# Kernel optimization log

Hardware: AMD Instinct MI355X
Metric: run time of the kernel (lower is better)

The kernel has to match this reference:

```python
import jax, jax.numpy as jnp
import numpy as np

N_NODES = 40000
EMB = 256
NHEADS = 2
HEAD = EMB // NHEADS
NLAYERS = 4
NGNN = 2
LN_EPS = 1e-5
LEAKY = 0.01


def setup_inputs() -> dict:
    key = jax.random.key(0)
    ks = iter(jax.random.split(key, 40))
    nrm = lambda shape, s=0.05: jax.random.normal(next(ks), shape, dtype=jnp.float32) * s
    inp = {
        'feat0': nrm((20000, 512), 1.0),
        'feat1': nrm((20000, 512), 1.0),
        'fc_w0': nrm((256, 512)), 'fc_b0': jnp.zeros((256,), jnp.float32),
        'fc_w1': nrm((256, 512)), 'fc_b1': jnp.zeros((256,), jnp.float32),
        'gcn_w': nrm((NGNN, 256, 256)),
        'edge_src': jax.random.randint(next(ks), (640000,), 0, N_NODES),
        'edge_dst': jax.random.randint(next(ks), (640000,), 0, N_NODES),
        'dg_seqs': jax.random.randint(next(ks), (1024, 64), 0, N_NODES),
        'pt_seqs': jax.random.randint(next(ks), (1024, 64), 0, N_NODES),
        'type_emb': nrm((4, 4), 1.0),
        'node_type': jax.random.randint(next(ks), (N_NODES,), 0, 4),
        'gt_wl': nrm((8, 256, 256)), 'gt_wr': nrm((8, 256, 256)),
        'gt_al': nrm((8, 1, HEAD)), 'gt_ar': nrm((8, 1, HEAD)),
        'gt_wf': nrm((8, 256, 256)),
        'ln_g': jnp.ones((8, 256), jnp.float32), 'ln_b': jnp.zeros((8, 256), jnp.float32),
        'proj_d_w': nrm((2, 256, 256)), 'proj_d_b': jnp.zeros((2, 256), jnp.float32),
        'proj_p_w': nrm((2, 256, 256)), 'proj_p_b': jnp.zeros((2, 256), jnp.float32),
        'ml_w1': nrm((256, 512)), 'ml_b1': jnp.zeros((256,), jnp.float32),
        'ml_w2': nrm((128, 256)), 'ml_b2': jnp.zeros((128,), jnp.float32),
        'ml_w3': nrm((1, 128)), 'ml_b3': jnp.zeros((1,), jnp.float32),
    }
    return inp


def _layernorm(x, g, b):
    m = x.mean(-1, keepdims=True)
    v = ((x - m) ** 2).mean(-1, keepdims=True)
    return (x - m) * jax.lax.rsqrt(v + LN_EPS) * g + b


def _leaky(x):
    return jnp.where(x >= 0, x, LEAKY * x)


def _agt_layer(h, wl, wr, al, ar, wf, g, b):
    # h: [B, L, EMB]; additive (GAT-style) attention, temper = 1.0
    B, L, _ = h.shape
    fl = (h @ wl.T).reshape(B, L, NHEADS, HEAD).transpose(0, 2, 1, 3)  # [B,H,L,hd]
    fr = (h @ wr.T).reshape(B, L, NHEADS, HEAD).transpose(0, 2, 1, 3)
    sl = _leaky(fl) @ al.T                     # [B,H,L,1]
    sr = _leaky(fr) @ ar.T                     # [B,H,L,1]
    score = jax.nn.softmax(sl + sr.transpose(0, 1, 3, 2), axis=-1)  # [B,H,L,L]
    ctx = score @ fr                           # [B,H,L,hd]
    h_sa = ctx.transpose(0, 2, 1, 3).reshape(B, L, EMB)
    return _layernorm(h + h_sa @ wf.T, g, b)


def _gcn(gh, W, src, dst):
    # DGL GraphConv norm='both', allow_zero_in_degree, activation=relu
    ones = jnp.ones(src.shape[0], gh.dtype)
    deg_out = jnp.clip(jax.ops.segment_sum(ones, src, num_segments=N_NODES), 1.0)
    deg_in = jnp.clip(jax.ops.segment_sum(ones, dst, num_segments=N_NODES), 1.0)
    x = gh * (deg_out ** -0.5)[:, None]
    x = x @ W
    agg = jax.ops.segment_sum(x[src], dst, num_segments=N_NODES)
    return jax.nn.relu(agg * (deg_in ** -0.5)[:, None])


def reference(feat0, feat1, fc_w0, fc_b0, fc_w1, fc_b1, gcn_w, edge_src, edge_dst,
              dg_seqs, pt_seqs, type_emb, node_type, gt_wl, gt_wr, gt_al, gt_ar,
              gt_wf, ln_g, ln_b, proj_d_w, proj_d_b, proj_p_w, proj_p_b,
              ml_w1, ml_b1, ml_w2, ml_b2, ml_w3, ml_b3):
    # per-type input projections, concatenated along node dim
    h0 = feat0 @ fc_w0.T + fc_b0
    h1 = feat1 @ fc_w1.T + fc_b1
    gh = jnp.concatenate([h0, h1], axis=0)  # [N, EMB]
    r = type_emb[node_type]                 # computed but unused downstream (faithful)
    for layer in range(NGNN):
        gh = _gcn(gh, gcn_w[layer], edge_src, edge_dst)
    # graph transformer per node type (dropout = identity in eval)
    embs = []
    for t, seqs in ((0, dg_seqs), (1, pt_seqs)):
        h = gh[seqs]                        # [B, L, EMB]
        _ = r[seqs]
        for l in range(NLAYERS):
            i = t * NLAYERS + l
            h = _agt_layer(h, gt_wl[i], gt_wr[i], gt_al[i], gt_ar[i], gt_wf[i], ln_g[i], ln_b[i])
        embs.append(h[:, 0, :])
    dg_emb, pt_emb = embs
    # Proj heads: linear -> elu -> linear
    dg_emb = jax.nn.elu(dg_emb @ proj_d_w[0].T + proj_d_b[0]) @ proj_d_w[1].T + proj_d_b[1]
    pt_emb = jax.nn.elu(pt_emb @ proj_p_w[0].T + proj_p_b[0]) @ proj_p_w[1].T + proj_p_b[1]
    # Predict MLP on concat
    x = jnp.concatenate([dg_emb, pt_emb], axis=1)  # [B, 512]
    x = jax.nn.relu(x @ ml_w1.T + ml_b1)
    x = jax.nn.relu(x @ ml_w2.T + ml_b2)
    out = jax.nn.sigmoid(x @ ml_w3.T + ml_b3)
    return out.reshape(x.shape[0])
```

## Files before the change

### kernel.cpp

```cpp
#include <hip/hip_runtime.h>
#include <hip/hip_bf16.h>
#include <math.h>

typedef unsigned int u32;
typedef unsigned short u16;
typedef __attribute__((ext_vector_type(8))) short bf16x8;
typedef __attribute__((ext_vector_type(4))) float f32x4;

__device__ __forceinline__ float b2f(u16 u) { union { u32 i; float f; } c; c.i = ((u32)u) << 16; return c.f; }
__device__ __forceinline__ u16 f2b(float f) { __hip_bfloat16 h = __float2bfloat16(f); u16 r; __builtin_memcpy(&r, &h, 2); return r; }
__device__ __forceinline__ float b2f_lo(u32 w) { union { u32 i; float f; } c; c.i = w << 16; return c.f; }
__device__ __forceinline__ float b2f_hi(u32 w) { union { u32 i; float f; } c; c.i = w & 0xffff0000u; return c.f; }
__device__ __forceinline__ u32 pk2(float a, float b) { return (u32)f2b(a) | ((u32)f2b(b) << 16); }

__device__ __forceinline__ float wave_sum(float v) {
    #pragma unroll
    for (int off = 32; off > 0; off >>= 1) v += __shfl_xor(v, off, 64);
    return v;
}

template<int CTRL>
__device__ __forceinline__ float dpp_addf(float v) {
    int y = __builtin_amdgcn_update_dpp(0, __builtin_bit_cast(int, v), CTRL, 0xF, 0xF, true);
    return v + __builtin_bit_cast(float, y);
}
__device__ __forceinline__ float sum16_dpp(float v) {
    v = dpp_addf<0xB1>(v);
    v = dpp_addf<0x4E>(v);
    v = dpp_addf<0x141>(v);
    v = dpp_addf<0x140>(v);
    return v;
}
__device__ __forceinline__ float sum8_dpp(float v) {
    v = dpp_addf<0xB1>(v);
    v = dpp_addf<0x4E>(v);
    v = dpp_addf<0x141>(v);
    return v;
}

template<bool AF32>
__global__ __launch_bounds__(256) void mfma_gemm_kernel(
    const void* __restrict__ Av, const u16* __restrict__ B,
    const float* __restrict__ bias, const float* __restrict__ rowscale,
    u16* __restrict__ Cb, int M, int N, int K,
    const void* __restrict__ Av1, const u16* __restrict__ B1,
    const float* __restrict__ bias1, u16* __restrict__ Cb1)
{
    if (blockIdx.z) { Av = Av1; B = B1; bias = bias1; Cb = Cb1; }
    __shared__ u16 lds[(64 + 128) * 64];
    const int tid = threadIdx.x;
    const int wid = tid >> 6, lane = tid & 63;
    const int wr = wid >> 1, wc = wid & 1;
    const int m0 = blockIdx.y * 64, n0 = blockIdx.x * 128;

    f32x4 acc[2][4] = {};

    for (int k0 = 0; k0 < K; k0 += 64) {
        #pragma unroll
        for (int s = 0; s < 2; ++s) {
            int idx = tid + s * 256;
            int row = idx >> 3, g = idx & 7;
            int row_g = m0 + row; if (row_g >= M) row_g = M - 1;
            int swz = ((g << 4) ^ ((row & 7) << 4));
            if (AF32) {
                const float* src = (const float*)Av + (size_t)row_g * K + k0 + g * 8;
                float4 v0 = *(const float4*)src;
                float4 v1 = *(const float4*)(src + 4);
                uint4 pk;
                pk.x = pk2(v0.x, v0.y); pk.y = pk2(v0.z, v0.w);
                pk.z = pk2(v1.x, v1.y); pk.w = pk2(v1.z, v1.w);
                *(uint4*)((char*)lds + row * 128 + swz) = pk;
            } else {
                f32x4 v = *(const f32x4*)((const u16*)Av + (size_t)row_g * K + k0 + g * 8);
                *(f32x4*)((char*)lds + row * 128 + swz) = v;
            }
        }
        #pragma unroll
        for (int s = 0; s < 4; ++s) {
            int idx = tid + s * 256;
            int row = idx >> 3, g = idx & 7;
            int row_g = n0 + row; if (row_g >= N) row_g = N - 1;
            f32x4 v = *(const f32x4*)(B + (size_t)row_g * K + k0 + g * 8);
            *(f32x4*)((char*)lds + 8192 + row * 128 + ((g << 4) ^ ((row & 7) << 4))) = v;
        }
        __syncthreads();
        #pragma unroll
        for (int ks = 0; ks < 2; ++ks) {
            const int off = (ks * 64 + ((lane >> 4) << 4)) ^ ((lane & 7) << 4);
            const int ra = lane & 15;
            bf16x8 af[2], bfr[4];
            #pragma unroll
            for (int i = 0; i < 2; ++i)
                af[i] = *(bf16x8*)((char*)lds + (wr * 32 + i * 16 + ra) * 128 + off);
            #pragma unroll
            for (int j = 0; j < 4; ++j)
                bfr[j] = *(bf16x8*)((char*)lds + 8192 + (wc * 64 + j * 16 + ra) * 128 + off);
            #pragma unroll
            for (int i = 0; i < 2; ++i)
                #pragma unroll
                for (int j = 0; j < 4; ++j)
                    acc[i][j] = __builtin_amdgcn_mfma_f32_16x16x32_bf16(af[i], bfr[j], acc[i][j], 0, 0, 0);
        }
        __syncthreads();
    }

    const int cr = lane >> 4, ccol = lane & 15;
    #pragma unroll
    for (int i = 0; i < 2; ++i) {
        #pragma unroll
        for (int j = 0; j < 4; ++j) {
            int colg = n0 + wc * 64 + j * 16 + ccol;
            if (colg >= N) continue;
            float badd = bias ? bias[colg] : 0.f;
            #pragma unroll
            for (int reg = 0; reg < 4; ++reg) {
                int rowg = m0 + wr * 32 + i * 16 + cr * 4 + reg;
                if (rowg >= M) continue;
                float v = acc[i][j][reg] + badd;
                if (rowscale) v *= rowscale[rowg];
                Cb[(size_t)rowg * N + colg] = f2b(v);
            }
        }
    }
}

__global__ __launch_bounds__(512, 4) void fused_transformer_kernel(
    const float* __restrict__ gh, const int* __restrict__ dg_seqs,
    const int* __restrict__ pt_seqs,
    const u16* __restrict__ wrN,
    const u32* __restrict__ wfT2,
    const float* __restrict__ ar,
    const float* __restrict__ lng, const float* __restrict__ lnb,
    float* __restrict__ embT)
{
    __shared__ u16 ldsA[64 * 256];
    __shared__ float scoreH[2][64];
    __shared__ float ctxS[256];
    __shared__ float uS[2][256];

    const int tid = threadIdx.x;
    const int bx = blockIdx.x;
    const int t = bx >> 10, s = bx & 1023;
    const int r = tid >> 3, o8 = tid & 7;
    const int wid = tid >> 6, lane = tid & 63;
    const int hd = wid >> 2;
    const int g4 = lane >> 4, cl = lane & 15;

    const int* seqs = t ? pt_seqs : dg_seqs;

    float4 y[8];
    {
        int node = seqs[s * 64 + r];
        const float* src = gh + (size_t)node * 256 + o8 * 32;
        #pragma unroll
        for (int v = 0; v < 8; ++v) y[v] = *(const float4*)(src + v * 4);
    }

    for (int l = 0; l < 4; ++l) {
        const int li = t * 4 + l;
        {
            const int c = o8 >> 1, gb = (o8 & 1) * 4;
            #pragma unroll
            for (int gg = 0; gg < 4; ++gg) {
                float4 a = y[2 * gg], b = y[2 * gg + 1];
                uint4 pk;
                pk.x = pk2(a.x, a.y); pk.y = pk2(a.z, a.w);
                pk.z = pk2(b.x, b.y); pk.w = pk2(b.z, b.w);
                int g = gb + gg;
                *(uint4*)((char*)ldsA + c * 8192 + r * 128 + ((g << 4) ^ ((r & 7) << 4))) = pk;
            }
            if (tid < 128) ((float*)scoreH)[tid] = 0.f;
        }
        __syncthreads();

        f32x4 acc[4][2] = {};
        {
            const u16* wrl = wrN + (size_t)li * 65536;
            const int ra = lane & 15;
            #pragma unroll
            for (int kc = 0; kc < 8; ++kc) {
                const int c = kc >> 1, ks = kc & 1;
                const int off = (ks * 64 + ((lane >> 4) << 4)) ^ ((lane & 7) << 4);
                bf16x8 af[4], bfr[2];
                #pragma unroll
                for (int i = 0; i < 4; ++i)
                    af[i] = *(bf16x8*)((char*)ldsA + c * 8192 + (i * 16 + ra) * 128 + off);
                #pragma unroll
                for (int j = 0; j < 2; ++j)
                    bfr[j] = *(const bf16x8*)(wrl + ((size_t)((wid * 2 + j) * 8 + kc) << 9) + lane * 8);
                #pragma unroll
                for (int i = 0; i < 4; ++i)
                    #pragma unroll
                    for (int j = 0; j < 2; ++j)
                        acc[i][j] = __builtin_amdgcn_mfma_f32_16x16x32_bf16(af[i], bfr[j], acc[i][j], 0, 0, 0);
            }
        }

        {
            const float* arl = ar + li * 128;
            float arj[2];
            #pragma unroll
            for (int j = 0; j < 2; ++j) arj[j] = arl[(wid & 3) * 32 + j * 16 + cl];
            #pragma unroll
            for (int i = 0; i < 4; ++i)
                #pragma unroll
                for (int reg = 0; reg < 4; ++reg) {
                    float sc;
                    {
                        float x0 = acc[i][0][reg], x1 = acc[i][1][reg];
                        sc = (x0 >= 0.f ? x0 : 0.01f * x0) * arj[0]
                           + (x1 >= 0.f ? x1 : 0.01f * x1) * arj[1];
                    }
                    sc = sum16_dpp(sc);
                    if (cl == 0) atomicAdd(&scoreH[hd][i * 16 + g4 * 4 + reg], sc);
                }
        }
        __syncthreads();

        float p[4][4];
        {
            const float* sc = scoreH[hd];
            #pragma unroll
            for (int i = 0; i < 4; ++i)
                *(float4*)p[i] = *(const float4*)(sc + i * 16 + g4 * 4);
            float mx = -1e30f;
            #pragma unroll
            for (int i = 0; i < 4; ++i)
                #pragma unroll
                for (int reg = 0; reg < 4; ++reg) mx = fmaxf(mx, p[i][reg]);
            mx = fmaxf(mx, __shfl_xor(mx, 16, 64));
            mx = fmaxf(mx, __shfl_xor(mx, 32, 64));
            float sme = 0.f;
            #pragma unroll
            for (int i = 0; i < 4; ++i)
                #pragma unroll
                for (int reg = 0; reg < 4; ++reg) {
                    p[i][reg] = __expf(p[i][reg] - mx);
                    sme += p[i][reg];
                }
            sme += __shfl_xor(sme, 16, 64);
            sme += __shfl_xor(sme, 32, 64);
            float inv = 1.f / sme;
            #pragma unroll
            for (int i = 0; i < 4; ++i)
                #pragma unroll
                for (int reg = 0; reg < 4; ++reg) p[i][reg] *= inv;
        }

        {
            #pragma unroll
            for (int j = 0; j < 2; ++j) {
                float c = 0.f;
                #pragma unroll
                for (int i = 0; i < 4; ++i)
                    #pragma unroll
                    for (int reg = 0; reg < 4; ++reg)
                        c = fmaf(p[i][reg], acc[i][j][reg], c);
                c += __shfl_xor(c, 16, 64);
                c += __shfl_xor(c, 32, 64);
                if (g4 == 0) ctxS[wid * 32 + j * 16 + cl] = c;
            }
        }
        __syncthreads();

        {
            const int n = tid & 255, half = tid >> 8;
            const u32* wp = wfT2 + (size_t)li * 32768 + (size_t)half * 16384 + n;
            const float* cx = ctxS + half * 128;
            float ua0 = 0.f, ua1 = 0.f, ua2 = 0.f, ua3 = 0.f;
            #pragma unroll 4
            for (int d2 = 0; d2 < 64; d2 += 4) {
                u32 w0 = wp[(size_t)(d2 + 0) * 256];
                u32 w1 = wp[(size_t)(d2 + 1) * 256];
                u32 w2 = wp[(size_t)(d2 + 2) * 256];
                u32 w3 = wp[(size_t)(d2 + 3) * 256];
                ua0 = fmaf(cx[2 * d2 + 0], b2f_lo(w0), ua0);
                ua0 = fmaf(cx[2 * d2 + 1], b2f_hi(w0), ua0);
                ua1 = fmaf(cx[2 * d2 + 2], b2f_lo(w1), ua1);
                ua1 = fmaf(cx[2 * d2 + 3], b2f_hi(w1), ua1);
                ua2 = fmaf(cx[2 * d2 + 4], b2f_lo(w2), ua2);
                ua2 = fmaf(cx[2 * d2 + 5], b2f_hi(w2), ua2);
                ua3 = fmaf(cx[2 * d2 + 6], b2f_lo(w3), ua3);
                ua3 = fmaf(cx[2 * d2 + 7], b2f_hi(w3), ua3);
            }
            uS[half][n] = (ua0 + ua1) + (ua2 + ua3);
        }
        __syncthreads();

        {
            #pragma unroll
            for (int v = 0; v < 8; ++v) {
                int c0 = o8 * 32 + v * 4;
                float4 u0 = *(const float4*)&uS[0][c0];
                float4 u1 = *(const float4*)&uS[1][c0];
                y[v].x += u0.x + u1.x; y[v].y += u0.y + u1.y;
                y[v].z += u0.z + u1.z; y[v].w += u0.w + u1.w;
            }
            float sm = 0.f, qq = 0.f;
            #pragma unroll
            for (int v = 0; v < 8; ++v) {
                sm += y[v].x + y[v].y + y[v].z + y[v].w;
                qq += y[v].x * y[v].x + y[v].y * y[v].y + y[v].z * y[v].z + y[v].w * y[v].w;
            }
            sm = sum8_dpp(sm);
            qq = sum8_dpp(qq);
            float mean = sm * (1.f / 256.f);
            float var = qq * (1.f / 256.f) - mean * mean;
            float inv = rsqrtf(var + 1e-5f);
            const float* gl = lng + li * 256 + o8 * 32;
            const float* bl = lnb + li * 256 + o8 * 32;
            if (l < 3) {
                #pragma unroll
                for (int v = 0; v < 8; ++v) {
                    float4 gv = *(const float4*)(gl + v * 4);
                    float4 bv = *(const float4*)(bl + v * 4);
                    y[v].x = (y[v].x - mean) * inv * gv.x + bv.x;
                    y[v].y = (y[v].y - mean) * inv * gv.y + bv.y;
                    y[v].z = (y[v].z - mean) * inv * gv.z + bv.z;
                    y[v].w = (y[v].w - mean) * inv * gv.w + bv.w;
                }
            } else if (r == 0) {
                float* dst = embT + (size_t)(t * 1024 + s) * 256 + o8 * 32;
                #pragma unroll
                for (int v = 0; v < 8; ++v) {
                    float4 gv = *(const float4*)(gl + v * 4);
                    float4 bv = *(const float4*)(bl + v * 4);
                    float4 o;
                    o.x = (y[v].x - mean) * inv * gv.x + bv.x;
                    o.y = (y[v].y - mean) * inv * gv.y + bv.y;
                    o.z = (y[v].z - mean) * inv * gv.z + bv.z;
                    o.w = (y[v].w - mean) * inv * gv.w + bv.w;
                    *(float4*)(dst + v * 4) = o;
                }
            }
        }
    }
}

template<bool BT>
__global__ __launch_bounds__(256) void gemm_kernel(
    const float* __restrict__ A, const float* __restrict__ B,
    const float* __restrict__ bias, const float* __restrict__ rowscale,
    float* __restrict__ C,
    int M, int N, int K, int lda, int ldb, int ldc, int coff, int act,
    const float* __restrict__ A1, const float* __restrict__ B1,
    const float* __restrict__ bias1, float* __restrict__ C1, int coff1)
{
    if (blockIdx.z) { A = A1; B = B1; bias = bias1; C = C1; coff = coff1; }
    __shared__ float As[32][64 + 4];
    __shared__ float Bs[32][64 + 4];
    const int tid = threadIdx.x;
    const int m0 = blockIdx.y * 64;
    const int n0 = blockIdx.x * 64;
    const int ty = tid >> 4, tx = tid & 15;
    float acc[4][4] = {};
    for (int k0 = 0; k0 < K; k0 += 32) {
        #pragma unroll
        for (int r = 0; r < 2; ++r) {
            int f4 = tid + r * 256;
            int arw = f4 >> 3, af = (f4 & 7) << 2;
            float4 v = make_float4(0.f, 0.f, 0.f, 0.f);
            int grow = m0 + arw;
            if (grow < M) {
                v = *(const float4*)(A + (size_t)grow * lda + k0 + af);
                if (rowscale) { float s = rowscale[grow]; v.x *= s; v.y *= s; v.z *= s; v.w *= s; }
            }
            As[af + 0][arw] = v.x; As[af + 1][arw] = v.y; As[af + 2][arw] = v.z; As[af + 3][arw] = v.w;
        }
        #pragma unroll
        for (int r = 0; r < 2; ++r) {
            int f4 = tid + r * 256;
            int col = f4 >> 3, kf = (f4 & 7) << 2;
            float4 v = make_float4(0.f, 0.f, 0.f, 0.f);
            if (n0 + col < N) v = *(const float4*)(B + (size_t)(n0 + col) * ldb + k0 + kf);
            Bs[kf + 0][col] = v.x; Bs[kf + 1][col] = v.y; Bs[kf + 2][col] = v.z; Bs[kf + 3][col] = v.w;
        }
        __syncthreads();
        #pragma unroll
        for (int kk = 0; kk < 32; ++kk) {
            float4 a4 = *(const float4*)&As[kk][ty << 2];
            float4 b4 = *(const float4*)&Bs[kk][tx << 2];
            float a[4] = {a4.x, a4.y, a4.z, a4.w};
            float b[4] = {b4.x, b4.y, b4.z, b4.w};
            #pragma unroll
            for (int i = 0; i < 4; ++i)
                #pragma unroll
                for (int j = 0; j < 4; ++j)
                    acc[i][j] = fmaf(a[i], b[j], acc[i][j]);
        }
        __syncthreads();
    }
    #pragma unroll
    for (int i = 0; i < 4; ++i) {
        int row = m0 + (ty << 2) + i;
        if (row >= M) continue;
        #pragma unroll
        for (int j = 0; j < 4; ++j) {
            int col = n0 + (tx << 2) + j;
            if (col >= N) continue;
            float v = acc[i][j];
            if (bias) v += bias[col];
            if (act == 1) v = fmaxf(v, 0.f);
            else if (act == 2) v = (v > 0.f) ? v : expm1f(v);
            C[(size_t)row * ldc + coff + col] = v;
        }
    }
}

__global__ __launch_bounds__(256) void conv_flat_kernel(const float* __restrict__ in, u16* __restrict__ out, int n) {
    int i = (blockIdx.x * 256 + threadIdx.x) * 4;
    if (i >= n) return;
    float4 v = *(const float4*)(in + i);
    *(uint2*)(out + i) = make_uint2(pk2(v.x, v.y), pk2(v.z, v.w));
}
__global__ __launch_bounds__(256) void conv_gcnw_kernel(const float* __restrict__ w, u16* __restrict__ out) {
    int idx = blockIdx.x * 256 + threadIdx.x;
    int l = blockIdx.y;
    int k = idx >> 8, n = idx & 255;
    out[(size_t)l * 65536 + n * 256 + k] = f2b(w[(size_t)l * 65536 + k * 256 + n]);
}
__global__ __launch_bounds__(256) void conv_wrN_kernel(const float* __restrict__ w, u16* __restrict__ out) {
    int idx = blockIdx.x * 256 + threadIdx.x;
    int lane = idx & 63;
    int kc = (idx >> 6) & 7;
    int gn = (idx >> 9) & 15;
    int l = idx >> 13;
    int row = gn * 16 + (lane & 15);
    int k0 = kc * 32 + (lane >> 4) * 8;
    const float* src = w + ((size_t)l * 256 + row) * 256 + k0;
    float4 v0 = *(const float4*)src;
    float4 v1 = *(const float4*)(src + 4);
    uint4 pk;
    pk.x = pk2(v0.x, v0.y); pk.y = pk2(v0.z, v0.w);
    pk.z = pk2(v1.x, v1.y); pk.w = pk2(v1.z, v1.w);
    *(uint4*)(out + (size_t)idx * 8) = pk;
}
__global__ __launch_bounds__(256) void conv_wfT2_kernel(const float* __restrict__ w, u32* __restrict__ out) {
    int idx = blockIdx.x * 256 + threadIdx.x;
    int n = idx & 255;
    int d2 = (idx >> 8) & 127;
    int l = idx >> 15;
    const float* src = w + ((size_t)l * 256 + n) * 256 + 2 * d2;
    out[idx] = pk2(src[0], src[1]);
}

#define EDGE_CAP 128
__global__ __launch_bounds__(256) void bucket_fill_kernel(
    const int* __restrict__ src, const int* __restrict__ dst,
    int* __restrict__ ebuf, int* __restrict__ cursor, int* __restrict__ cnt_out, int ne)
{
    int e0 = (blockIdx.x * 256 + threadIdx.x) * 4;
    if (e0 >= ne) return;
    int4 s4 = *(const int4*)(src + e0);
    int4 d4 = *(const int4*)(dst + e0);
    atomicAdd(&cnt_out[s4.x], 1);
    atomicAdd(&cnt_out[s4.y], 1);
    atomicAdd(&cnt_out[s4.z], 1);
    atomicAdd(&cnt_out[s4.w], 1);
    int p0 = atomicAdd(&cursor[d4.x], 1);
    int p1 = atomicAdd(&cursor[d4.y], 1);
    int p2 = atomicAdd(&cursor[d4.z], 1);
    int p3 = atomicAdd(&cursor[d4.w], 1);
    if (p0 < EDGE_CAP) ebuf[(size_t)d4.x * EDGE_CAP + p0] = s4.x;
    if (p1 < EDGE_CAP) ebuf[(size_t)d4.y * EDGE_CAP + p1] = s4.y;
    if (p2 < EDGE_CAP) ebuf[(size_t)d4.z * EDGE_CAP + p2] = s4.z;
    if (p3 < EDGE_CAP) ebuf[(size_t)d4.w * EDGE_CAP + p3] = s4.w;
}
__global__ __launch_bounds__(256) void deg_fin_kernel(const int* __restrict__ cnt, float* __restrict__ dinv, int n) {
    int i = blockIdx.x * 256 + threadIdx.x;
    if (i < n) dinv[i] = rsqrtf(fmaxf((float)cnt[i], 1.0f));
}

template<bool WF, bool WB>
__global__ __launch_bounds__(256) void csr_agg_kernel(
    const u16* __restrict__ x, const int* __restrict__ ebuf,
    const int* __restrict__ deg, float* __restrict__ outf, u16* __restrict__ outb, int nnodes)
{
    int n = blockIdx.x * 4 + (threadIdx.x >> 6);
    if (n >= nnodes) return;
    int lane = threadIdx.x & 63;
    int d = deg[n];
    float dinv = rsqrtf(fmaxf((float)d, 1.0f));
    if (d > EDGE_CAP) d = EDGE_CAP;
    const int* eb = ebuf + (size_t)n * EDGE_CAP;
    const int co = lane << 2;
    float a0 = 0.f, a1 = 0.f, a2 = 0.f, a3 = 0.f;
    int k = 0;
    for (; k + 4 <= d; k += 4) {
        int4 s4 = *(const int4*)(eb + k);
        uint2 va = *(const uint2*)(x + (size_t)s4.x * 256 + co);
        uint2 vb = *(const uint2*)(x + (size_t)s4.y * 256 + co);
        uint2 vc = *(const uint2*)(x + (size_t)s4.z * 256 + co);
        uint2 vd = *(const uint2*)(x + (size_t)s4.w * 256 + co);
        a0 += b2f_lo(va.x) + b2f_lo(vb.x) + b2f_lo(vc.x) + b2f_lo(vd.x);
        a1 += b2f_hi(va.x) + b2f_hi(vb.x) + b2f_hi(vc.x) + b2f_hi(vd.x);
        a2 += b2f_lo(va.y) + b2f_lo(vb.y) + b2f_lo(vc.y) + b2f_lo(vd.y);
        a3 += b2f_hi(va.y) + b2f_hi(vb.y) + b2f_hi(vc.y) + b2f_hi(vd.y);
    }
    for (; k < d; ++k) {
        int s = eb[k];
        uint2 v = *(const uint2*)(x + (size_t)s * 256 + co);
        a0 += b2f_lo(v.x); a1 += b2f_hi(v.x);
        a2 += b2f_lo(v.y); a3 += b2f_hi(v.y);
    }
    a0 = fmaxf(a0 * dinv, 0.f); a1 = fmaxf(a1 * dinv, 0.f);
    a2 = fmaxf(a2 * dinv, 0.f); a3 = fmaxf(a3 * dinv, 0.f);
    if (WF) *(float4*)(outf + (size_t)n * 256 + co) = make_float4(a0, a1, a2, a3);
    if (WB) *(uint2*)(outb + (size_t)n * 256 + co) = make_uint2(pk2(a0, a1), pk2(a2, a3));
}

__global__ __launch_bounds__(256) void final_kernel(
    const float* __restrict__ m2, const float* __restrict__ w3,
    const float* __restrict__ b3, float* __restrict__ out, int nrows)
{
    int row = blockIdx.x * 4 + (threadIdx.x >> 6);
    int lane = threadIdx.x & 63;
    if (row >= nrows) return;
    float s = m2[(size_t)row * 128 + lane] * w3[lane]
            + m2[(size_t)row * 128 + 64 + lane] * w3[64 + lane];
    s = wave_sum(s);
    if (lane == 0) out[row] = 1.f / (1.f + expf(-(s + b3[0])));
}

static inline int cdiv(int a, int b) { return (a + b - 1) / b; }

extern "C" void kernel_launch(void* const* d_in, const int* in_sizes, int n_in,
                              void* d_out, int out_size, void* d_ws, size_t ws_size,
                              hipStream_t stream)
{
    const float* feat0   = (const float*)d_in[0];
    const float* feat1   = (const float*)d_in[1];
    const float* fc_w0   = (const float*)d_in[2];
    const float* fc_b0   = (const float*)d_in[3];
    const float* fc_w1   = (const float*)d_in[4];
    const float* fc_b1   = (const float*)d_in[5];
    const float* gcn_w   = (const float*)d_in[6];
    const int*   edge_src= (const int*)d_in[7];
    const int*   edge_dst= (const int*)d_in[8];
    const int*   dg_seqs = (const int*)d_in[9];
    const int*   pt_seqs = (const int*)d_in[10];
    const float* gt_wr   = (const float*)d_in[14];
    const float* gt_ar   = (const float*)d_in[16];
    const float* gt_wf   = (const float*)d_in[17];
    const float* ln_g    = (const float*)d_in[18];
    const float* ln_b    = (const float*)d_in[19];
    const float* proj_d_w= (const float*)d_in[20];
    const float* proj_d_b= (const float*)d_in[21];
    const float* proj_p_w= (const float*)d_in[22];
    const float* proj_p_b= (const float*)d_in[23];
    const float* ml_w1   = (const float*)d_in[24];
    const float* ml_b1   = (const float*)d_in[25];
    const float* ml_w2   = (const float*)d_in[26];
    const float* ml_b2   = (const float*)d_in[27];
    const float* ml_w3   = (const float*)d_in[28];
    const float* ml_b3   = (const float*)d_in[29];
    float* out = (float*)d_out;

    float* base  = (float*)d_ws;
    float* gh    = base;
    float* gcnR  = gh + 10240000;
    float* dego  = gcnR + 15440000;
    float* embT  = dego + 40000;
    float* t1    = embT + 524288;
    float* mx    = t1 + 524288;
    float* m1    = mx + 524288;
    float* m2    = m1 + 262144;
    float* wreg  = m2 + 131072;

    u16* tmp_b   = (u16*)gcnR;
    int* ebuf    = (int*)(gcnR + 5120000);
    int* cursor  = ebuf + (size_t)40000 * EDGE_CAP;
    int* cnt_out = cursor + 40000;
    u16* gh_b    = (u16*)(gcnR + 10320000);

    u16* fcw_b   = (u16*)wreg;
    u16* gcnw_b  = fcw_b + 262144;
    u16* wrN     = gcnw_b + 131072;
    u32* wfT2    = (u32*)(wrN + 524288);

    conv_flat_kernel<<<cdiv(131072 / 4, 256), 256, 0, stream>>>(fc_w0, fcw_b, 131072);
    conv_flat_kernel<<<cdiv(131072 / 4, 256), 256, 0, stream>>>(fc_w1, fcw_b + 131072, 131072);
    conv_gcnw_kernel<<<dim3(256, 2), 256, 0, stream>>>(gcn_w, gcnw_b);
    conv_wrN_kernel<<<256, 256, 0, stream>>>(gt_wr, wrN);
    conv_wfT2_kernel<<<1024, 256, 0, stream>>>(gt_wf, wfT2);

    mfma_gemm_kernel<true><<<dim3(2, cdiv(20000, 64), 2), 256, 0, stream>>>(
        feat0, fcw_b, fc_b0, nullptr, gh_b, 20000, 256, 512,
        feat1, fcw_b + 131072, fc_b1, gh_b + (size_t)20000 * 256);

    hipMemsetAsync(cursor, 0, 80000 * sizeof(int), stream);
    bucket_fill_kernel<<<625, 256, 0, stream>>>(edge_src, edge_dst, ebuf, cursor, cnt_out, 640000);
    deg_fin_kernel<<<cdiv(40000, 256), 256, 0, stream>>>(cnt_out, dego, 40000);

    mfma_gemm_kernel<false><<<dim3(2, cdiv(40000, 64), 1), 256, 0, stream>>>(
        gh_b, gcnw_b, nullptr, dego, tmp_b, 40000, 256, 256,
        gh_b, gcnw_b, nullptr, tmp_b);
    csr_agg_kernel<false, true><<<10000, 256, 0, stream>>>(tmp_b, ebuf, cursor, gh, gh_b, 40000);
    mfma_gemm_kernel<false><<<dim3(2, cdiv(40000, 64), 1), 256, 0, stream>>>(
        gh_b, gcnw_b + 65536, nullptr, dego, tmp_b, 40000, 256, 256,
        gh_b, gcnw_b, nullptr, tmp_b);
    csr_agg_kernel<true, false><<<10000, 256, 0, stream>>>(tmp_b, ebuf, cursor, gh, gh_b, 40000);

    fused_transformer_kernel<<<2048, 512, 0, stream>>>(
        gh, dg_seqs, pt_seqs, wrN, wfT2, gt_ar, ln_g, ln_b, embT);

    gemm_kernel<true><<<dim3(4, 16, 2), 256, 0, stream>>>(
        embT, proj_d_w, proj_d_b, nullptr, t1, 1024, 256, 256, 256, 256, 256, 0, 2,
        embT + 262144, proj_p_w, proj_p_b, t1 + 262144, 0);
    gemm_kernel<true><<<dim3(4, 16, 2), 256, 0, stream>>>(
        t1, proj_d_w + 65536, proj_d_b + 256, nullptr, mx, 1024, 256, 256, 256, 256, 512, 0, 0,
        t1 + 262144, proj_p_w + 65536, proj_p_b + 256, mx, 256);

    gemm_kernel<true><<<dim3(4, 16, 1), 256, 0, stream>>>(
        mx, ml_w1, ml_b1, nullptr, m1, 1024, 256, 512, 512, 512, 256, 0, 1,
        mx, ml_w1, ml_b1, m1, 0);
    gemm_kernel<true><<<dim3(2, 16, 1), 256, 0, stream>>>(
        m1, ml_w2, ml_b2, nullptr, m2, 1024, 128, 256, 256, 256, 128, 0, 1,
        m1, ml_w2, ml_b2, m2, 0);
    final_kernel<<<256, 256, 0, stream>>>(m2, ml_w3, ml_b3, out, 1024);
}
```

Measured before the change: 651.1 us.

## Prefetch Wf weights, reswizzle LDS, merge conversion kernels, fuse MLP tail

The transformer kernel now prefetches the first 16 Wf weight words into registers at the start of each layer, so the loads overlap the QK/MFMA phase. It also adds a chunk-dependent XOR to the LDS swizzle and reads the context vector with float4 loads. Separately, five weight-conversion launches are merged into one kernel, and the last MLP GEMM and the sigmoid kernel are fused into a single tail kernel. These changes cut launch overhead and load latency at the cost of more register pressure in the main kernel.

```diff
diff --git a/kernel.cpp b/kernel.cpp
--- a/kernel.cpp
+++ b/kernel.cpp
@@ -147,6 +147,7 @@
     const int g4 = lane >> 4, cl = lane & 15;
 
     const int* seqs = t ? pt_seqs : dg_seqs;
+    const int un = tid & 255, uhalf = tid >> 8;
 
     float4 y[8];
     {
@@ -158,6 +159,12 @@
 
     for (int l = 0; l < 4; ++l) {
         const int li = t * 4 + l;
+        const u32* wp = wfT2 + (size_t)li * 32768 + (size_t)uhalf * 16384 + un;
+
+        u32 wpre[16];
+        #pragma unroll
+        for (int i = 0; i < 16; ++i) wpre[i] = wp[(size_t)i * 256];
+
         {
             const int c = o8 >> 1, gb = (o8 & 1) * 4;
             #pragma unroll
@@ -167,7 +174,8 @@
                 pk.x = pk2(a.x, a.y); pk.y = pk2(a.z, a.w);
                 pk.z = pk2(b.x, b.y); pk.w = pk2(b.z, b.w);
                 int g = gb + gg;
-                *(uint4*)((char*)ldsA + c * 8192 + r * 128 + ((g << 4) ^ ((r & 7) << 4))) = pk;
+                int off = ((g << 4) ^ ((r & 7) << 4)) ^ (c << 4);
+                *(uint4*)((char*)ldsA + c * 8192 + r * 128 + off) = pk;
             }
             if (tid < 128) ((float*)scoreH)[tid] = 0.f;
         }
@@ -180,7 +188,7 @@
             #pragma unroll
             for (int kc = 0; kc < 8; ++kc) {
                 const int c = kc >> 1, ks = kc & 1;
-                const int off = (ks * 64 + ((lane >> 4) << 4)) ^ ((lane & 7) << 4);
+                const int off = ((ks * 64 + ((lane >> 4) << 4)) ^ ((lane & 7) << 4)) ^ (c << 4);
                 bf16x8 af[4], bfr[2];
                 #pragma unroll
                 for (int i = 0; i < 4; ++i)
@@ -264,26 +272,31 @@
         __syncthreads();
 
         {
-            const int n = tid & 255, half = tid >> 8;
-            const u32* wp = wfT2 + (size_t)li * 32768 + (size_t)half * 16384 + n;
-            const float* cx = ctxS + half * 128;
+            const float* cx = ctxS + uhalf * 128;
             float ua0 = 0.f, ua1 = 0.f, ua2 = 0.f, ua3 = 0.f;
-            #pragma unroll 4
+            #pragma unroll
             for (int d2 = 0; d2 < 64; d2 += 4) {
-                u32 w0 = wp[(size_t)(d2 + 0) * 256];
-                u32 w1 = wp[(size_t)(d2 + 1) * 256];
-                u32 w2 = wp[(size_t)(d2 + 2) * 256];
-                u32 w3 = wp[(size_t)(d2 + 3) * 256];
-                ua0 = fmaf(cx[2 * d2 + 0], b2f_lo(w0), ua0);
-                ua0 = fmaf(cx[2 * d2 + 1], b2f_hi(w0), ua0);
-                ua1 = fmaf(cx[2 * d2 + 2], b2f_lo(w1), ua1);
-                ua1 = fmaf(cx[2 * d2 + 3], b2f_hi(w1), ua1);
-                ua2 = fmaf(cx[2 * d2 + 4], b2f_lo(w2), ua2);
-                ua2 = fmaf(cx[2 * d2 + 5], b2f_hi(w2), ua2);
-                ua3 = fmaf(cx[2 * d2 + 6], b2f_lo(w3), ua3);
-                ua3 = fmaf(cx[2 * d2 + 7], b2f_hi(w3), ua3);
-            }
-            uS[half][n] = (ua0 + ua1) + (ua2 + ua3);
+                u32 w0, w1, w2, w3;
+                if (d2 < 16) {
+                    w0 = wpre[d2]; w1 = wpre[d2 + 1]; w2 = wpre[d2 + 2]; w3 = wpre[d2 + 3];
+                } else {
+                    w0 = wp[(size_t)(d2 + 0) * 256];
+                    w1 = wp[(size_t)(d2 + 1) * 256];
+                    w2 = wp[(size_t)(d2 + 2) * 256];
+                    w3 = wp[(size_t)(d2 + 3) * 256];
+                }
+                float4 c0 = *(const float4*)(cx + 2 * d2);
+                float4 c1 = *(const float4*)(cx + 2 * d2 + 4);
+                ua0 = fmaf(c0.x, b2f_lo(w0), ua0);
+                ua0 = fmaf(c0.y, b2f_hi(w0), ua0);
+                ua1 = fmaf(c0.z, b2f_lo(w1), ua1);
+                ua1 = fmaf(c0.w, b2f_hi(w1), ua1);
+                ua2 = fmaf(c1.x, b2f_lo(w2), ua2);
+                ua2 = fmaf(c1.y, b2f_hi(w2), ua2);
+                ua3 = fmaf(c1.z, b2f_lo(w3), ua3);
+                ua3 = fmaf(c1.w, b2f_hi(w3), ua3);
+            }
+            uS[uhalf][un] = (ua0 + ua1) + (ua2 + ua3);
         }
         __syncthreads();
 
@@ -407,41 +420,48 @@
     }
 }
 
-__global__ __launch_bounds__(256) void conv_flat_kernel(const float* __restrict__ in, u16* __restrict__ out, int n) {
-    int i = (blockIdx.x * 256 + threadIdx.x) * 4;
-    if (i >= n) return;
-    float4 v = *(const float4*)(in + i);
-    *(uint2*)(out + i) = make_uint2(pk2(v.x, v.y), pk2(v.z, v.w));
-}
-__global__ __launch_bounds__(256) void conv_gcnw_kernel(const float* __restrict__ w, u16* __restrict__ out) {
-    int idx = blockIdx.x * 256 + threadIdx.x;
-    int l = blockIdx.y;
-    int k = idx >> 8, n = idx & 255;
-    out[(size_t)l * 65536 + n * 256 + k] = f2b(w[(size_t)l * 65536 + k * 256 + n]);
-}
-__global__ __launch_bounds__(256) void conv_wrN_kernel(const float* __restrict__ w, u16* __restrict__ out) {
-    int idx = blockIdx.x * 256 + threadIdx.x;
-    int lane = idx & 63;
-    int kc = (idx >> 6) & 7;
-    int gn = (idx >> 9) & 15;
-    int l = idx >> 13;
-    int row = gn * 16 + (lane & 15);
-    int k0 = kc * 32 + (lane >> 4) * 8;
-    const float* src = w + ((size_t)l * 256 + row) * 256 + k0;
-    float4 v0 = *(const float4*)src;
-    float4 v1 = *(const float4*)(src + 4);
-    uint4 pk;
-    pk.x = pk2(v0.x, v0.y); pk.y = pk2(v0.z, v0.w);
-    pk.z = pk2(v1.x, v1.y); pk.w = pk2(v1.z, v1.w);
-    *(uint4*)(out + (size_t)idx * 8) = pk;
-}
-__global__ __launch_bounds__(256) void conv_wfT2_kernel(const float* __restrict__ w, u32* __restrict__ out) {
-    int idx = blockIdx.x * 256 + threadIdx.x;
-    int n = idx & 255;
-    int d2 = (idx >> 8) & 127;
-    int l = idx >> 15;
-    const float* src = w + ((size_t)l * 256 + n) * 256 + 2 * d2;
-    out[idx] = pk2(src[0], src[1]);
+__global__ __launch_bounds__(256) void conv_all_kernel(
+    const float* __restrict__ fc_w0, const float* __restrict__ fc_w1,
+    const float* __restrict__ gcn_w, const float* __restrict__ gt_wr,
+    const float* __restrict__ gt_wf,
+    u16* __restrict__ fcw_b, u16* __restrict__ gcnw_b,
+    u16* __restrict__ wrN, u32* __restrict__ wfT2)
+{
+    int bid = blockIdx.x, tid = threadIdx.x;
+    if (bid < 256) {
+        const float* src = bid < 128 ? fc_w0 : fc_w1;
+        u16* dst = fcw_b + (bid < 128 ? 0 : 131072);
+        int i = ((bid & 127) * 256 + tid) * 4;
+        float4 v = *(const float4*)(src + i);
+        *(uint2*)(dst + i) = make_uint2(pk2(v.x, v.y), pk2(v.z, v.w));
+    } else if (bid < 768) {
+        int idx = (bid - 256) * 256 + tid;
+        int l = idx >> 16, rem = idx & 65535;
+        int k = rem >> 8, n = rem & 255;
+        gcnw_b[(size_t)l * 65536 + n * 256 + k] = f2b(gcn_w[(size_t)l * 65536 + k * 256 + n]);
+    } else if (bid < 1024) {
+        int idx = (bid - 768) * 256 + tid;
+        int lane = idx & 63;
+        int kc = (idx >> 6) & 7;
+        int gn = (idx >> 9) & 15;
+        int l = idx >> 13;
+        int row = gn * 16 + (lane & 15);
+        int k0 = kc * 32 + (lane >> 4) * 8;
+        const float* src = gt_wr + ((size_t)l * 256 + row) * 256 + k0;
+        float4 v0 = *(const float4*)src;
+        float4 v1 = *(const float4*)(src + 4);
+        uint4 pk;
+        pk.x = pk2(v0.x, v0.y); pk.y = pk2(v0.z, v0.w);
+        pk.z = pk2(v1.x, v1.y); pk.w = pk2(v1.z, v1.w);
+        *(uint4*)(wrN + (size_t)idx * 8) = pk;
+    } else {
+        int idx = (bid - 1024) * 256 + tid;
+        int n = idx & 255;
+        int d2 = (idx >> 8) & 127;
+        int l = idx >> 15;
+        const float* src = gt_wf + ((size_t)l * 256 + n) * 256 + 2 * d2;
+        wfT2[idx] = pk2(src[0], src[1]);
+    }
 }
 
 #define EDGE_CAP 128
@@ -509,15 +529,32 @@
     if (WB) *(uint2*)(outb + (size_t)n * 256 + co) = make_uint2(pk2(a0, a1), pk2(a2, a3));
 }
 
-__global__ __launch_bounds__(256) void final_kernel(
-    const float* __restrict__ m2, const float* __restrict__ w3,
-    const float* __restrict__ b3, float* __restrict__ out, int nrows)
-{
-    int row = blockIdx.x * 4 + (threadIdx.x >> 6);
-    int lane = threadIdx.x & 63;
-    if (row >= nrows) return;
-    float s = m2[(size_t)row * 128 + lane] * w3[lane]
-            + m2[(size_t)row * 128 + 64 + lane] * w3[64 + lane];
+__global__ __launch_bounds__(256) void mlp_tail_kernel(
+    const float* __restrict__ m1, const float* __restrict__ w2,
+    const float* __restrict__ b2, const float* __restrict__ w3,
+    const float* __restrict__ b3, float* __restrict__ out)
+{
+    __shared__ float rowS[4][256];
+    const int w = threadIdx.x >> 6, lane = threadIdx.x & 63;
+    const int row = blockIdx.x * 4 + w;
+    *(float4*)&rowS[w][lane * 4] = *(const float4*)(m1 + (size_t)row * 256 + lane * 4);
+    __syncthreads();
+    const float* rp = rowS[w];
+    float v0 = b2[lane], v1 = b2[64 + lane];
+    const float* wa = w2 + (size_t)lane * 256;
+    const float* wb = w2 + (size_t)(64 + lane) * 256;
+    #pragma unroll 8
+    for (int d = 0; d < 256; d += 4) {
+        float4 rv = *(const float4*)(rp + d);
+        float4 a = *(const float4*)(wa + d);
+        float4 b = *(const float4*)(wb + d);
+        v0 = fmaf(rv.x, a.x, v0); v0 = fmaf(rv.y, a.y, v0);
+        v0 = fmaf(rv.z, a.z, v0); v0 = fmaf(rv.w, a.w, v0);
+        v1 = fmaf(rv.x, b.x, v1); v1 = fmaf(rv.y, b.y, v1);
+        v1 = fmaf(rv.z, b.z, v1); v1 = fmaf(rv.w, b.w, v1);
+    }
+    v0 = fmaxf(v0, 0.f); v1 = fmaxf(v1, 0.f);
+    float s = v0 * w3[lane] + v1 * w3[64 + lane];
     s = wave_sum(s);
     if (lane == 0) out[row] = 1.f / (1.f + expf(-(s + b3[0])));
 }
@@ -578,11 +615,8 @@
     u16* wrN     = gcnw_b + 131072;
     u32* wfT2    = (u32*)(wrN + 524288);
 
-    conv_flat_kernel<<<cdiv(131072 / 4, 256), 256, 0, stream>>>(fc_w0, fcw_b, 131072);
-    conv_flat_kernel<<<cdiv(131072 / 4, 256), 256, 0, stream>>>(fc_w1, fcw_b + 131072, 131072);
-    conv_gcnw_kernel<<<dim3(256, 2), 256, 0, stream>>>(gcn_w, gcnw_b);
-    conv_wrN_kernel<<<256, 256, 0, stream>>>(gt_wr, wrN);
-    conv_wfT2_kernel<<<1024, 256, 0, stream>>>(gt_wf, wfT2);
+    conv_all_kernel<<<2048, 256, 0, stream>>>(
+        fc_w0, fc_w1, gcn_w, gt_wr, gt_wf, fcw_b, gcnw_b, wrN, wfT2);
 
     mfma_gemm_kernel<true><<<dim3(2, cdiv(20000, 64), 2), 256, 0, stream>>>(
         feat0, fcw_b, fc_b0, nullptr, gh_b, 20000, 256, 512,
@@ -614,8 +648,5 @@
     gemm_kernel<true><<<dim3(4, 16, 1), 256, 0, stream>>>(
         mx, ml_w1, ml_b1, nullptr, m1, 1024, 256, 512, 512, 512, 256, 0, 1,
         mx, ml_w1, ml_b1, m1, 0);
-    gemm_kernel<true><<<dim3(2, 16, 1), 256, 0, stream>>>(
-        m1, ml_w2, ml_b2, nullptr, m2, 1024, 128, 256, 256, 256, 128, 0, 1,
-        m1, ml_w2, ml_b2, m2, 0);
-    final_kernel<<<256, 256, 0, stream>>>(m2, ml_w3, ml_b3, out, 1024);
-}
+    mlp_tail_kernel<<<256, 256, 0, stream>>>(m1, ml_w2, ml_b2, ml_w3, ml_b3, out);
+}
```

Result: slower. 724.7 us (+11.3%).
